# Kernel optimization log

Measured on AMD Instinct MI355X. Metric: run time of the kernel, lower is better.

The kernel has to match this reference:

```python
import jax, jax.numpy as jnp
import numpy as np

HIDDEN = 1024
N_HEADS = 16
HEAD_DIM = HIDDEN // N_HEADS
B, S = 4, 4096


def setup_inputs() -> dict:
    key = jax.random.key(0)
    k1, k2, k3, k4, k5 = jax.random.split(key, 5)
    hidden_states = jax.random.normal(k1, (B, S, HIDDEN), dtype=jnp.float32)
    attention_mask = jnp.zeros((B, 1, 1, S), dtype=jnp.float32)
    scale = 1.0 / np.sqrt(HIDDEN)
    Wq = jax.random.normal(k2, (HIDDEN, HIDDEN), dtype=jnp.float32) * scale
    bq = jax.random.normal(k3, (HIDDEN,), dtype=jnp.float32) * 0.01
    Wkv = jax.random.normal(k4, (HIDDEN, HIDDEN), dtype=jnp.float32) * scale
    bkv = jax.random.normal(k5, (HIDDEN,), dtype=jnp.float32) * 0.01
    return {"hidden_states": hidden_states, "attention_mask": attention_mask,
            "Wq": Wq, "bq": bq, "Wkv": Wkv, "bkv": bkv}


def _split_heads(x, b, s):
    # [B, S, HIDDEN] -> [B, H, S, D]
    return x.reshape(b, s, N_HEADS, HEAD_DIM).transpose(0, 2, 1, 3)


def reference(hidden_states, attention_mask, Wq, bq, Wkv, bkv):
    b, s, _ = hidden_states.shape
    inv_sqrt_d = 1.0 / np.sqrt(HEAD_DIM)

    q = _split_heads(hidden_states @ Wq + bq, b, s)     # [B,H,S,D]
    k = _split_heads(hidden_states @ Wkv + bkv, b, s)   # [B,H,S,D]; value == key

    # ---- global token (index 0) attends to everything ----
    gq = q[:, :, 0:1, :]                                              # [B,H,1,D]
    g_scores = jnp.einsum('bhqd,bhkd->bhqk', gq, k) * inv_sqrt_d + attention_mask
    g_attn = jax.nn.softmax(g_scores, axis=-1)                        # [B,H,1,S]
    g_vec = jnp.einsum('bhqk,bhkd->bhqd', g_attn, k)                  # [B,H,1,D]

    # ---- local tokens 1..S-1: keys = [self, global_vec, prev, next(wrap to 0)] ----
    k_self = k[:, :, 1:, :]                                           # [B,H,S-1,D]
    k_glob = jnp.broadcast_to(g_vec, k_self.shape)                    # [B,H,S-1,D]
    k_prev = k[:, :, :-1, :]                                          # [B,H,S-1,D]
    k_next = jnp.concatenate([k[:, :, 2:, :], k[:, :, 0:1, :]], axis=2)
    keys4 = jnp.stack([k_self, k_glob, k_prev, k_next], axis=-1)      # [B,H,S-1,D,4]

    l_scores = jnp.einsum('bhsd,bhsdk->bhsk', q[:, :, 1:, :], keys4) * inv_sqrt_d
    l_attn = jax.nn.softmax(l_scores, axis=-1)                        # [B,H,S-1,4]
    l_vec = jnp.einsum('bhsk,bhsdk->bhsd', l_attn, keys4)             # [B,H,S-1,D]

    context = jnp.concatenate([g_vec, l_vec], axis=2)                 # [B,H,S,D]
    context = context.transpose(0, 2, 1, 3).reshape(b, s, N_HEADS * HEAD_DIM)
    return context, l_attn[:, :, :, None, :]                          # [B,H,S-1,1,4]
```

## Files before the change

### kernel.cpp

```cpp
#include <hip/hip_runtime.h>
#include <hip/hip_bf16.h>

#define NHEADS 16
#define HDIM   64
#define HID    1024
#define BB     4
#define SS     4096
#define MM     (BB*SS)
#define KK     HID
#define NN     (2*HID)

using short8 = __attribute__((ext_vector_type(8))) short;
using f32x4  = __attribute__((ext_vector_type(4))) float;

__device__ __forceinline__ float bf2f(ushort u) {
  return __uint_as_float(((unsigned)u) << 16);
}
__device__ __forceinline__ ushort f2bf(float f) {
  unsigned u = __float_as_uint(f);
  unsigned r = (u + 0x7fffu + ((u >> 16) & 1u)) >> 16;
  return (ushort)r;
}

__device__ __forceinline__ void gload16(const void* g, void* l) {
  __builtin_amdgcn_global_load_lds(
      (const __attribute__((address_space(1))) void*)g,
      (__attribute__((address_space(3))) void*)l, 16, 0, 0);
}

__global__ __launch_bounds__(256) void cast_hs_k(const float* __restrict__ in,
                                                 ushort* __restrict__ out) {
  size_t i = ((size_t)blockIdx.x * 256 + threadIdx.x) * 8;
  float4 a = *(const float4*)(in + i);
  float4 b = *(const float4*)(in + i + 4);
  ushort r[8];
  r[0]=f2bf(a.x); r[1]=f2bf(a.y); r[2]=f2bf(a.z); r[3]=f2bf(a.w);
  r[4]=f2bf(b.x); r[5]=f2bf(b.y); r[6]=f2bf(b.z); r[7]=f2bf(b.w);
  *(uint4*)(out + i) = *(const uint4*)r;
}

__global__ __launch_bounds__(256) void wcast_k(const float* __restrict__ Wq,
                                               const float* __restrict__ Wkv,
                                               ushort* __restrict__ Bt) {
  __shared__ float tile[32][33];
  int k0 = blockIdx.x * 32, n0 = blockIdx.y * 32;
  int tx = threadIdx.x, ty = threadIdx.y;
  const float* src = (n0 < HID) ? Wq : Wkv;
  int nc = (n0 < HID) ? n0 : n0 - HID;
#pragma unroll
  for (int j = 0; j < 4; ++j)
    tile[ty + 8*j][tx] = src[(size_t)(k0 + ty + 8*j) * HID + nc + tx];
  __syncthreads();
#pragma unroll
  for (int j = 0; j < 4; ++j)
    Bt[(size_t)(n0 + ty + 8*j) * KK + k0 + tx] = f2bf(tile[tx][ty + 8*j]);
}

__global__ __launch_bounds__(512, 2) void gemm_k(const ushort* __restrict__ A,
                                                 const ushort* __restrict__ Bt,
                                                 const float* __restrict__ bq,
                                                 const float* __restrict__ bkv,
                                                 ushort* __restrict__ C) {
  extern __shared__ char lds_c[];
  const int tid = threadIdx.x;
  const int bid = blockIdx.x;
  const int wg = (bid & 7) * 64 + (bid >> 3);
  const int tm = wg >> 3, tn = wg & 7;
  const int w = tid >> 6, lane = tid & 63;
  const int wr = w >> 2, wc = w & 3;
  const int lr = lane & 15, hi = lane >> 4;

  const ushort* Ab = A  + (size_t)tm * 256 * KK;
  const ushort* Bb = Bt + (size_t)tn * 256 * KK;

  const int d0 = tid * 16;
  const int gch = (tid & 3) ^ ((tid >> 3) & 3);
  const size_t soff0 = (size_t)(tid >> 2) * KK + gch * 8;
  const size_t soff1 = soff0 + (size_t)128 * KK;

  const int swz = (hi ^ ((lr >> 1) & 3)) << 4;
  const int arow = (wr * 128 + lr) * 64 + swz;
  const int brow = (wc * 64 + lr) * 64 + swz;

  f32x4 acc[8][4];
#pragma unroll
  for (int M = 0; M < 8; ++M)
#pragma unroll
    for (int n = 0; n < 4; ++n) acc[M][n] = (f32x4){0.f, 0.f, 0.f, 0.f};
  short8 bfrag[4];

#define STG(PANEL, KOFF, DSTB)                                                  \
  {                                                                             \
    const ushort* g_ = (PANEL) + (KOFF);                                        \
    gload16(g_ + soff0, lds_c + (DSTB) + d0);                                   \
    gload16(g_ + soff1, lds_c + (DSTB) + 8192 + d0);                            \
  }

#define LOADB(BBASE)                                                            \
  _Pragma("unroll") for (int n = 0; n < 4; ++n)                                 \
    bfrag[n] = *(const short8*)(lds_c + (BBASE) + n * 1024 + brow);

#define WAITV(N)                                                                \
  { asm volatile("s_waitcnt vmcnt(" #N ")" ::: "memory");                       \
    __builtin_amdgcn_sched_barrier(0); }

#define PH(ABASE, MH, STAGE_CODE, TAIL_CODE)                                    \
  {                                                                             \
    short8 afrag[4];                                                            \
    _Pragma("unroll") for (int m = 0; m < 4; ++m)                               \
      afrag[m] = *(const short8*)(lds_c + (ABASE) + (MH) * 4096 +               \
                                  m * 1024 + arow);                             \
    STAGE_CODE;                                                                 \
    __builtin_amdgcn_s_barrier();                                               \
    __builtin_amdgcn_sched_barrier(0);     \
    __builtin_amdgcn_s_setprio(1);                                              \
    _Pragma("unroll") for (int m = 0; m < 4; ++m)                               \
      _Pragma("unroll") for (int n = 0; n < 4; ++n)                             \
        acc[(MH) * 4 + m][n] = __builtin_amdgcn_mfma_f32_16x16x32_bf16(         \
            bfrag[n], afrag[m], acc[(MH) * 4 + m][n], 0, 0, 0);                 \
    __builtin_amdgcn_s_setprio(0);                                              \
    TAIL_CODE;                                                                  \
    __builtin_amdgcn_s_barrier();                                               \
    asm volatile("" ::: "memory");                                              \
  }

  STG(Bb, 0,   32768);
  STG(Ab, 0,   0);
  STG(Bb, 32,  49152);
  STG(Ab, 32,  16384);
  STG(Bb, 64,  98304);
  STG(Ab, 64,  65536);
  WAITV(8)
  __builtin_amdgcn_s_barrier();
  asm volatile("" ::: "memory");

#pragma unroll 1
  for (int it = 0; it < 7; ++it) {
    LOADB(32768)
    PH(0, 0, STG(Bb, (2 * it + 1) * 64 + 32, 114688), {})
    PH(0, 1, STG(Ab, (2 * it + 1) * 64 + 32, 81920), WAITV(8))
    LOADB(49152)
    PH(16384, 0, STG(Bb, (2 * it + 2) * 64, 32768), {})
    PH(16384, 1, STG(Ab, (2 * it + 2) * 64, 0), WAITV(8))
    LOADB(98304)
    PH(65536, 0, STG(Bb, (2 * it + 2) * 64 + 32, 49152), {})
    PH(65536, 1, STG(Ab, (2 * it + 2) * 64 + 32, 16384), WAITV(8))
    LOADB(114688)
    PH(81920, 0, STG(Bb, (2 * it + 3) * 64, 98304), {})
    PH(81920, 1, STG(Ab, (2 * it + 3) * 64, 65536), WAITV(8))
  }
  LOADB(32768)
  PH(0, 0, STG(Bb, 15 * 64 + 32, 114688), {})
  PH(0, 1, STG(Ab, 15 * 64 + 32, 81920), WAITV(8))
  LOADB(49152)
  PH(16384, 0, {}, {})
  PH(16384, 1, {}, WAITV(4))
  LOADB(98304)
  PH(65536, 0, {}, {})
  PH(65536, 1, {}, WAITV(0))
  LOADB(114688)
  PH(81920, 0, {}, {})
  PH(81920, 1, {}, {})

#undef PH
#undef WAITV
#undef LOADB
#undef STG

  const float* bias = (tn < 4) ? (bq + tn * 256) : (bkv + (tn - 4) * 256);
  float4 bv[4];
#pragma unroll
  for (int n = 0; n < 4; ++n)
    bv[n] = *(const float4*)(bias + wc * 64 + n * 16 + hi * 4);

#pragma unroll
  for (int M = 0; M < 8; ++M) {
    size_t row = (size_t)tm * 256 + wr * 128 + M * 16 + lr;
    ushort* cp = C + row * NN + tn * 256 + wc * 64 + hi * 4;
#pragma unroll
    for (int n = 0; n < 4; ++n) {
      unsigned p0 = (unsigned)f2bf(acc[M][n][0] + bv[n].x) |
                    ((unsigned)f2bf(acc[M][n][1] + bv[n].y) << 16);
      unsigned p1 = (unsigned)f2bf(acc[M][n][2] + bv[n].z) |
                    ((unsigned)f2bf(acc[M][n][3] + bv[n].w) << 16);
      uint2 st; st.x = p0; st.y = p1;
      *(uint2*)(cp + n * 16) = st;
    }
  }
}

#define GCH 8
#define GCS (SS / GCH)

__global__ __launch_bounds__(512) void gattn_part_k(const ushort* __restrict__ QK,
                                                    const float* __restrict__ mask,
                                                    float* __restrict__ P) {
  const int bh = blockIdx.x >> 3, c = blockIdx.x & 7;
  const int b = bh >> 4, h = bh & 15;
  const int tid = threadIdx.x, w = tid >> 6, lane = tid & 63;
  __shared__ float sc[GCS];
  __shared__ float red[8];
  __shared__ float vacc[8][64];

  const float gq = bf2f(QK[(size_t)b * SS * NN + h * HDIM + lane]);
  const int s0 = c * GCS;
  float mx = -1e30f;
  for (int s = w; s < GCS; s += 8) {
    float kv = bf2f(QK[((size_t)b * SS + s0 + s) * NN + HID + h * HDIM + lane]);
    float p = gq * kv;
#pragma unroll
    for (int o = 32; o; o >>= 1) p += __shfl_xor(p, o, 64);
    p = p * 0.125f + mask[b * SS + s0 + s];
    if (lane == 0) sc[s] = p;
    mx = fmaxf(mx, p);
  }
  if (lane == 0) red[w] = mx;
  __syncthreads();
  float bm = -1e30f;
#pragma unroll
  for (int i = 0; i < 8; ++i) bm = fmaxf(bm, red[i]);
  __syncthreads();
  float ls = 0.f;
  for (int s = tid; s < GCS; s += 512) {
    float e = __expf(sc[s] - bm);
    sc[s] = e;
    ls += e;
  }
#pragma unroll
  for (int o = 32; o; o >>= 1) ls += __shfl_xor(ls, o, 64);
  if (lane == 0) red[w] = ls;
  __syncthreads();
  float tot = 0.f;
#pragma unroll
  for (int i = 0; i < 8; ++i) tot += red[i];

  float a = 0.f;
  for (int s = w; s < GCS; s += 8)
    a += sc[s] * bf2f(QK[((size_t)b * SS + s0 + s) * NN + HID + h * HDIM + lane]);
  vacc[w][lane] = a;
  __syncthreads();
  if (w == 0) {
    float v = 0.f;
#pragma unroll
    for (int i = 0; i < 8; ++i) v += vacc[i][lane];
    P[1024 + (bh * 8 + c) * 64 + lane] = v;
    if (lane == 0) {
      P[bh * 8 + c] = bm;
      P[512 + bh * 8 + c] = tot;
    }
  }
}

__global__ __launch_bounds__(64) void gattn_comb_k(const float* __restrict__ P,
                                                   float* __restrict__ ctx,
                                                   float* __restrict__ gvec) {
  const int bh = blockIdx.x, b = bh >> 4, h = bh & 15;
  const int lane = threadIdx.x;
  float pm[8];
  float m = -1e30f;
#pragma unroll
  for (int c = 0; c < 8; ++c) { pm[c] = P[bh * 8 + c]; m = fmaxf(m, pm[c]); }
  float tot = 0.f, g = 0.f;
#pragma unroll
  for (int c = 0; c < 8; ++c) {
    float e = __expf(pm[c] - m);
    tot += P[512 + bh * 8 + c] * e;
    g += P[1024 + (bh * 8 + c) * 64 + lane] * e;
  }
  g /= tot;
  gvec[b * HID + h * HDIM + lane] = g;
  ctx[(size_t)b * SS * HID + h * HDIM + lane] = g;
}

__device__ __forceinline__ void unpack16(const ushort* __restrict__ p, float* f) {
  uint4 v0 = *(const uint4*)p;
  uint4 v1 = *(const uint4*)(p + 8);
  unsigned u[8] = {v0.x, v0.y, v0.z, v0.w, v1.x, v1.y, v1.z, v1.w};
#pragma unroll
  for (int i = 0; i < 8; ++i) {
    f[2*i]   = __uint_as_float(u[i] << 16);
    f[2*i+1] = __uint_as_float(u[i] & 0xffff0000u);
  }
}

__global__ __launch_bounds__(256) void local_attn_k(const ushort* __restrict__ QK,
                                                    const float* __restrict__ gvec,
                                                    float* __restrict__ out) {
  const int blk = blockIdx.x;
  const int b = blk >> 10;
  const int s = 1 + ((blk & 1023) << 2) + (int)(threadIdx.x >> 6);
  if (s >= SS) return;
  const int lane = threadIdx.x & 63;
  const int g = lane >> 2, j = lane & 3;
  const int db = g*HDIM + j*16;

  const size_t base = ((size_t)b*SS + s) * NN;
  const ushort* qp  = QK + base + db;
  const ushort* ksp = QK + base + HID + db;
  const ushort* kpp = QK + base - NN + HID + db;
  const int sn = (s == SS-1) ? 0 : s + 1;
  const ushort* knp = QK + ((size_t)b*SS + sn)*NN + HID + db;
  const float*  gvp = gvec + b*HID + db;

  float q[16], ks[16], kp[16], kn[16], gv[16];
  unpack16(qp, q); unpack16(ksp, ks); unpack16(kpp, kp); unpack16(knp, kn);
#pragma unroll
  for (int t = 0; t < 16; t += 4) *(float4*)(gv + t) = *(const float4*)(gvp + t);

  float d0=0.f, d1=0.f, d2=0.f, d3=0.f;
#pragma unroll
  for (int t = 0; t < 16; ++t) {
    d0 += q[t]*ks[t]; d1 += q[t]*gv[t]; d2 += q[t]*kp[t]; d3 += q[t]*kn[t];
  }
  d0 += __shfl_xor(d0, 1, 64); d0 += __shfl_xor(d0, 2, 64);
  d1 += __shfl_xor(d1, 1, 64); d1 += __shfl_xor(d1, 2, 64);
  d2 += __shfl_xor(d2, 1, 64); d2 += __shfl_xor(d2, 2, 64);
  d3 += __shfl_xor(d3, 1, 64); d3 += __shfl_xor(d3, 2, 64);

  float s0 = d0*0.125f, s1 = d1*0.125f, s2 = d2*0.125f, s3 = d3*0.125f;
  float m = fmaxf(fmaxf(s0, s1), fmaxf(s2, s3));
  float e0 = __expf(s0 - m), e1 = __expf(s1 - m), e2 = __expf(s2 - m), e3 = __expf(s3 - m);
  float inv = 1.f / (e0 + e1 + e2 + e3);
  float a0 = e0*inv, a1 = e1*inv, a2 = e2*inv, a3 = e3*inv;

  float o[16];
#pragma unroll
  for (int t = 0; t < 16; ++t) o[t] = a0*ks[t] + a1*gv[t] + a2*kp[t] + a3*kn[t];
  float* cp = out + ((size_t)b*SS + s)*HID + db;
#pragma unroll
  for (int t = 0; t < 16; t += 4) *(float4*)(cp + t) = *(const float4*)(o + t);

  if (j == 0) {
    float4 av; av.x = a0; av.y = a1; av.z = a2; av.w = a3;
    *(float4*)(out + (size_t)BB*SS*HID + (((size_t)b*NHEADS + g)*(SS-1) + (s-1))*4) = av;
  }
}

extern "C" void kernel_launch(void* const* d_in, const int* in_sizes, int n_in,
                              void* d_out, int out_size, void* d_ws, size_t ws_size,
                              hipStream_t stream) {
  const float* hs   = (const float*)d_in[0];
  const float* mask = (const float*)d_in[1];
  const float* Wq   = (const float*)d_in[2];
  const float* bq   = (const float*)d_in[3];
  const float* Wkv  = (const float*)d_in[4];
  const float* bkv  = (const float*)d_in[5];
  float* out = (float*)d_out;

  char* ws = (char*)d_ws;
  ushort* hsb  = (ushort*)ws;
  ushort* Bt   = (ushort*)(ws + 33554432);
  ushort* QK   = (ushort*)(ws + 33554432 + 4194304);
  float*  gvec = (float*)(ws + 33554432 + 4194304 + 67108864);
  float*  P    = (float*)(ws + 33554432 + 4194304 + 67108864 + 16384);

  cast_hs_k<<<MM*KK/(256*8), 256, 0, stream>>>(hs, hsb);
  wcast_k<<<dim3(KK/32, NN/32), dim3(32, 8), 0, stream>>>(Wq, Wkv, Bt);
  gemm_k<<<dim3((MM/256)*(NN/256)), dim3(512), 131072, stream>>>(hsb, Bt, bq, bkv, QK);
  gattn_part_k<<<BB*NHEADS*GCH, 512, 0, stream>>>(QK, mask, P);
  gattn_comb_k<<<BB*NHEADS, 64, 0, stream>>>(P, out, gvec);
  local_attn_k<<<BB*1024, 256, 0, stream>>>(QK, gvec, out);
}
```

Before: 176.1 us.

## Double-buffer GEMM LDS fragments, fuse cast kernels, cache keys in registers

```diff
diff --git a/kernel.cpp b/kernel.cpp
--- a/kernel.cpp
+++ b/kernel.cpp
@@ -28,32 +28,35 @@
       (__attribute__((address_space(3))) void*)l, 16, 0, 0);
 }
 
-__global__ __launch_bounds__(256) void cast_hs_k(const float* __restrict__ in,
-                                                 ushort* __restrict__ out) {
-  size_t i = ((size_t)blockIdx.x * 256 + threadIdx.x) * 8;
-  float4 a = *(const float4*)(in + i);
-  float4 b = *(const float4*)(in + i + 4);
-  ushort r[8];
-  r[0]=f2bf(a.x); r[1]=f2bf(a.y); r[2]=f2bf(a.z); r[3]=f2bf(a.w);
-  r[4]=f2bf(b.x); r[5]=f2bf(b.y); r[6]=f2bf(b.z); r[7]=f2bf(b.w);
-  *(uint4*)(out + i) = *(const uint4*)r;
-}
-
-__global__ __launch_bounds__(256) void wcast_k(const float* __restrict__ Wq,
-                                               const float* __restrict__ Wkv,
-                                               ushort* __restrict__ Bt) {
+__global__ __launch_bounds__(256) void prep_k(const float* __restrict__ hs,
+                                              const float* __restrict__ Wq,
+                                              const float* __restrict__ Wkv,
+                                              ushort* __restrict__ hsb,
+                                              ushort* __restrict__ Bt) {
   __shared__ float tile[32][33];
-  int k0 = blockIdx.x * 32, n0 = blockIdx.y * 32;
-  int tx = threadIdx.x, ty = threadIdx.y;
-  const float* src = (n0 < HID) ? Wq : Wkv;
-  int nc = (n0 < HID) ? n0 : n0 - HID;
-#pragma unroll
-  for (int j = 0; j < 4; ++j)
-    tile[ty + 8*j][tx] = src[(size_t)(k0 + ty + 8*j) * HID + nc + tx];
-  __syncthreads();
-#pragma unroll
-  for (int j = 0; j < 4; ++j)
-    Bt[(size_t)(n0 + ty + 8*j) * KK + k0 + tx] = f2bf(tile[tx][ty + 8*j]);
+  const int blk = blockIdx.x, tid = threadIdx.x;
+  if (blk < 8192) {
+    size_t i = ((size_t)blk * 256 + tid) * 8;
+    float4 a = *(const float4*)(hs + i);
+    float4 b = *(const float4*)(hs + i + 4);
+    ushort r[8];
+    r[0]=f2bf(a.x); r[1]=f2bf(a.y); r[2]=f2bf(a.z); r[3]=f2bf(a.w);
+    r[4]=f2bf(b.x); r[5]=f2bf(b.y); r[6]=f2bf(b.z); r[7]=f2bf(b.w);
+    *(uint4*)(hsb + i) = *(const uint4*)r;
+  } else {
+    const int e = blk - 8192;
+    const int k0 = (e & 31) * 32, n0 = (e >> 5) * 32;
+    const int tx = tid & 31, ty = tid >> 5;
+    const float* src = (n0 < HID) ? Wq : Wkv;
+    const int nc = (n0 < HID) ? n0 : n0 - HID;
+#pragma unroll
+    for (int j = 0; j < 4; ++j)
+      tile[ty + 8*j][tx] = src[(size_t)(k0 + ty + 8*j) * HID + nc + tx];
+    __syncthreads();
+#pragma unroll
+    for (int j = 0; j < 4; ++j)
+      Bt[(size_t)(n0 + ty + 8*j) * KK + k0 + tx] = f2bf(tile[tx][ty + 8*j]);
+  }
 }
 
 __global__ __launch_bounds__(512, 2) void gemm_k(const ushort* __restrict__ A,
@@ -87,7 +90,8 @@
   for (int M = 0; M < 8; ++M)
 #pragma unroll
     for (int n = 0; n < 4; ++n) acc[M][n] = (f32x4){0.f, 0.f, 0.f, 0.f};
-  short8 bfrag[4];
+
+  short8 aX[4], aY[4], bX[4], bY[4];
 
 #define STG(PANEL, KOFF, DSTB)                                                  \
   {                                                                             \
@@ -96,30 +100,32 @@
     gload16(g_ + soff1, lds_c + (DSTB) + 8192 + d0);                            \
   }
 
-#define LOADB(BBASE)                                                            \
+#define RDA(DST, ABASE, MH)                                                     \
+  _Pragma("unroll") for (int m = 0; m < 4; ++m)                                 \
+    DST[m] = *(const short8*)(lds_c + (ABASE) + (MH) * 4096 + m * 1024 + arow);
+
+#define RDB(DST, BBASE)                                                         \
   _Pragma("unroll") for (int n = 0; n < 4; ++n)                                 \
-    bfrag[n] = *(const short8*)(lds_c + (BBASE) + n * 1024 + brow);
+    DST[n] = *(const short8*)(lds_c + (BBASE) + n * 1024 + brow);
 
 #define WAITV(N)                                                                \
   { asm volatile("s_waitcnt vmcnt(" #N ")" ::: "memory");                       \
     __builtin_amdgcn_sched_barrier(0); }
 
-#define PH(ABASE, MH, STAGE_CODE, TAIL_CODE)                                    \
+#define PHASE(AF, BF, MH, RD_CODE, STG_CODE, WAIT_CODE)                         \
   {                                                                             \
-    short8 afrag[4];                                                            \
-    _Pragma("unroll") for (int m = 0; m < 4; ++m)                               \
-      afrag[m] = *(const short8*)(lds_c + (ABASE) + (MH) * 4096 +               \
-                                  m * 1024 + arow);                             \
-    STAGE_CODE;                                                                 \
+    RD_CODE                                                                     \
+    __builtin_amdgcn_sched_barrier(0);                                          \
+    STG_CODE                                                                    \
     __builtin_amdgcn_s_barrier();                                               \
-    __builtin_amdgcn_sched_barrier(0);     \
+    __builtin_amdgcn_sched_barrier(0);                                          \
     __builtin_amdgcn_s_setprio(1);                                              \
     _Pragma("unroll") for (int m = 0; m < 4; ++m)                               \
       _Pragma("unroll") for (int n = 0; n < 4; ++n)                             \
         acc[(MH) * 4 + m][n] = __builtin_amdgcn_mfma_f32_16x16x32_bf16(         \
-            bfrag[n], afrag[m], acc[(MH) * 4 + m][n], 0, 0, 0);                 \
+            BF[n], AF[m], acc[(MH) * 4 + m][n], 0, 0, 0);                       \
     __builtin_amdgcn_s_setprio(0);                                              \
-    TAIL_CODE;                                                                  \
+    WAIT_CODE                                                                   \
     __builtin_amdgcn_s_barrier();                                               \
     asm volatile("" ::: "memory");                                              \
   }
@@ -130,41 +136,37 @@
   STG(Ab, 32,  16384);
   STG(Bb, 64,  98304);
   STG(Ab, 64,  65536);
-  WAITV(8)
+  WAITV(4)
   __builtin_amdgcn_s_barrier();
   asm volatile("" ::: "memory");
+  RDB(bX, 32768);
+  RDA(aX, 0, 0);
 
 #pragma unroll 1
   for (int it = 0; it < 7; ++it) {
-    LOADB(32768)
-    PH(0, 0, STG(Bb, (2 * it + 1) * 64 + 32, 114688), {})
-    PH(0, 1, STG(Ab, (2 * it + 1) * 64 + 32, 81920), WAITV(8))
-    LOADB(49152)
-    PH(16384, 0, STG(Bb, (2 * it + 2) * 64, 32768), {})
-    PH(16384, 1, STG(Ab, (2 * it + 2) * 64, 0), WAITV(8))
-    LOADB(98304)
-    PH(65536, 0, STG(Bb, (2 * it + 2) * 64 + 32, 49152), {})
-    PH(65536, 1, STG(Ab, (2 * it + 2) * 64 + 32, 16384), WAITV(8))
-    LOADB(114688)
-    PH(81920, 0, STG(Bb, (2 * it + 3) * 64, 98304), {})
-    PH(81920, 1, STG(Ab, (2 * it + 3) * 64, 65536), WAITV(8))
-  }
-  LOADB(32768)
-  PH(0, 0, STG(Bb, 15 * 64 + 32, 114688), {})
-  PH(0, 1, STG(Ab, 15 * 64 + 32, 81920), WAITV(8))
-  LOADB(49152)
-  PH(16384, 0, {}, {})
-  PH(16384, 1, {}, WAITV(4))
-  LOADB(98304)
-  PH(65536, 0, {}, {})
-  PH(65536, 1, {}, WAITV(0))
-  LOADB(114688)
-  PH(81920, 0, {}, {})
-  PH(81920, 1, {}, {})
-
-#undef PH
+    const int t1 = 2 * it + 1, t2 = 2 * it + 2, t3 = 2 * it + 3;
+    PHASE(aX, bX, 0, { RDA(aY, 0, 1); },                      STG(Bb, t1*64+32, 114688), WAITV(6))
+    PHASE(aY, bX, 1, { RDA(aX, 16384, 0); RDB(bY, 49152); },  STG(Ab, t1*64+32, 81920),  WAITV(6))
+    PHASE(aX, bY, 0, { RDA(aY, 16384, 1); },                  STG(Bb, t2*64, 32768),     WAITV(6))
+    PHASE(aY, bY, 1, { RDA(aX, 65536, 0); RDB(bX, 98304); },  STG(Ab, t2*64, 0),         WAITV(6))
+    PHASE(aX, bX, 0, { RDA(aY, 65536, 1); },                  STG(Bb, t2*64+32, 49152),  WAITV(6))
+    PHASE(aY, bX, 1, { RDA(aX, 81920, 0); RDB(bY, 114688); }, STG(Ab, t2*64+32, 16384),  WAITV(6))
+    PHASE(aX, bY, 0, { RDA(aY, 81920, 1); },                  STG(Bb, t3*64, 98304),     WAITV(6))
+    PHASE(aY, bY, 1, { RDA(aX, 0, 0); RDB(bX, 32768); },      STG(Ab, t3*64, 65536),     WAITV(6))
+  }
+  PHASE(aX, bX, 0, { RDA(aY, 0, 1); },                      STG(Bb, 15*64+32, 114688), WAITV(6))
+  PHASE(aY, bX, 1, { RDA(aX, 16384, 0); RDB(bY, 49152); },  STG(Ab, 15*64+32, 81920),  WAITV(6))
+  PHASE(aX, bY, 0, { RDA(aY, 16384, 1); },                  {}, WAITV(4))
+  PHASE(aY, bY, 1, { RDA(aX, 65536, 0); RDB(bX, 98304); },  {}, WAITV(2))
+  PHASE(aX, bX, 0, { RDA(aY, 65536, 1); },                  {}, WAITV(0))
+  PHASE(aY, bX, 1, { RDA(aX, 81920, 0); RDB(bY, 114688); }, {}, {})
+  PHASE(aX, bY, 0, { RDA(aY, 81920, 1); },                  {}, {})
+  PHASE(aY, bY, 1, {}, {}, {})
+
+#undef PHASE
 #undef WAITV
-#undef LOADB
+#undef RDB
+#undef RDA
 #undef STG
 
   const float* bias = (tn < 4) ? (bq + tn * 256) : (bkv + (tn - 4) * 256);
@@ -204,9 +206,13 @@
 
   const float gq = bf2f(QK[(size_t)b * SS * NN + h * HDIM + lane]);
   const int s0 = c * GCS;
+  float kvv[64];
   float mx = -1e30f;
-  for (int s = w; s < GCS; s += 8) {
+#pragma unroll
+  for (int i = 0; i < 64; ++i) {
+    const int s = w + i * 8;
     float kv = bf2f(QK[((size_t)b * SS + s0 + s) * NN + HID + h * HDIM + lane]);
+    kvv[i] = kv;
     float p = gq * kv;
 #pragma unroll
     for (int o = 32; o; o >>= 1) p += __shfl_xor(p, o, 64);
@@ -235,8 +241,8 @@
   for (int i = 0; i < 8; ++i) tot += red[i];
 
   float a = 0.f;
-  for (int s = w; s < GCS; s += 8)
-    a += sc[s] * bf2f(QK[((size_t)b * SS + s0 + s) * NN + HID + h * HDIM + lane]);
+#pragma unroll
+  for (int i = 0; i < 64; ++i) a += sc[w + i * 8] * kvv[i];
   vacc[w][lane] = a;
   __syncthreads();
   if (w == 0) {
@@ -354,8 +360,7 @@
   float*  gvec = (float*)(ws + 33554432 + 4194304 + 67108864);
   float*  P    = (float*)(ws + 33554432 + 4194304 + 67108864 + 16384);
 
-  cast_hs_k<<<MM*KK/(256*8), 256, 0, stream>>>(hs, hsb);
-  wcast_k<<<dim3(KK/32, NN/32), dim3(32, 8), 0, stream>>>(Wq, Wkv, Bt);
+  prep_k<<<8192 + 2048, 256, 0, stream>>>(hs, Wq, Wkv, hsb, Bt);
   gemm_k<<<dim3((MM/256)*(NN/256)), dim3(512), 131072, stream>>>(hsb, Bt, bq, bkv, QK);
   gattn_part_k<<<BB*NHEADS*GCH, 512, 0, stream>>>(QK, mask, P);
   gattn_comb_k<<<BB*NHEADS, 64, 0, stream>>>(P, out, gvec);
```

New measurement: 193.7 us. 10.0% more time.

## Shrink GEMM tiles to 128x128 and reuse neighbor keys in local attention

Applied to the files above, without the earlier changes.

```diff
diff --git a/kernel.cpp b/kernel.cpp
--- a/kernel.cpp
+++ b/kernel.cpp
@@ -56,7 +56,7 @@
     Bt[(size_t)(n0 + ty + 8*j) * KK + k0 + tx] = f2bf(tile[tx][ty + 8*j]);
 }
 
-__global__ __launch_bounds__(512, 2) void gemm_k(const ushort* __restrict__ A,
+__global__ __launch_bounds__(256, 2) void gemm_k(const ushort* __restrict__ A,
                                                  const ushort* __restrict__ Bt,
                                                  const float* __restrict__ bq,
                                                  const float* __restrict__ bkv,
@@ -64,125 +64,117 @@
   extern __shared__ char lds_c[];
   const int tid = threadIdx.x;
   const int bid = blockIdx.x;
-  const int wg = (bid & 7) * 64 + (bid >> 3);
-  const int tm = wg >> 3, tn = wg & 7;
+  const int wg = (bid & 7) * 256 + (bid >> 3);
+  const int tm = wg >> 4, tn = wg & 15;
   const int w = tid >> 6, lane = tid & 63;
-  const int wr = w >> 2, wc = w & 3;
+  const int wr = w >> 1, wc = w & 1;
   const int lr = lane & 15, hi = lane >> 4;
 
-  const ushort* Ab = A  + (size_t)tm * 256 * KK;
-  const ushort* Bb = Bt + (size_t)tn * 256 * KK;
-
-  const int d0 = tid * 16;
-  const int gch = (tid & 3) ^ ((tid >> 3) & 3);
-  const size_t soff0 = (size_t)(tid >> 2) * KK + gch * 8;
-  const size_t soff1 = soff0 + (size_t)128 * KK;
-
-  const int swz = (hi ^ ((lr >> 1) & 3)) << 4;
-  const int arow = (wr * 128 + lr) * 64 + swz;
-  const int brow = (wc * 64 + lr) * 64 + swz;
-
-  f32x4 acc[8][4];
-#pragma unroll
-  for (int M = 0; M < 8; ++M)
-#pragma unroll
-    for (int n = 0; n < 4; ++n) acc[M][n] = (f32x4){0.f, 0.f, 0.f, 0.f};
+  const ushort* Ab = A  + (size_t)tm * 128 * KK;
+  const ushort* Bb = Bt + (size_t)tn * 128 * KK;
+
+  int srow[4], scol[4];
+#pragma unroll
+  for (int i = 0; i < 4; ++i) {
+    int o = i * 4096 + tid * 16;
+    int row = o >> 7, ch = (o >> 4) & 7;
+    srow[i] = row;
+    scol[i] = ((ch ^ (row & 7)) << 3);
+  }
+
+  const int aoff0 = (wr * 64 + lr) * 128;
+  const int boff0 = (wc * 64 + lr) * 128;
+  const int r7 = lr & 7;
+
+  f32x4 acc[4][4];
+#pragma unroll
+  for (int m = 0; m < 4; ++m)
+#pragma unroll
+    for (int n = 0; n < 4; ++n) acc[m][n] = (f32x4){0.f, 0.f, 0.f, 0.f};
   short8 bfrag[4];
 
-#define STG(PANEL, KOFF, DSTB)                                                  \
+#define STGALL(T1, DSTB)                                                        \
   {                                                                             \
-    const ushort* g_ = (PANEL) + (KOFF);                                        \
-    gload16(g_ + soff0, lds_c + (DSTB) + d0);                                   \
-    gload16(g_ + soff1, lds_c + (DSTB) + 8192 + d0);                            \
-  }
-
-#define LOADB(BBASE)                                                            \
+    _Pragma("unroll") for (int i = 0; i < 4; ++i)                               \
+      gload16(Ab + (T1) * 64 + (size_t)srow[i] * KK + scol[i],                  \
+              lds_c + (DSTB) + i * 4096 + tid * 16);                            \
+    _Pragma("unroll") for (int i = 0; i < 4; ++i)                               \
+      gload16(Bb + (T1) * 64 + (size_t)srow[i] * KK + scol[i],                  \
+              lds_c + (DSTB) + 16384 + i * 4096 + tid * 16);                    \
+  }
+
+#define LOADB(BBASE, CB)                                                        \
   _Pragma("unroll") for (int n = 0; n < 4; ++n)                                 \
-    bfrag[n] = *(const short8*)(lds_c + (BBASE) + n * 1024 + brow);
+    bfrag[n] = *(const short8*)(lds_c + (BBASE) + boff0 + n * 2048 +            \
+                                ((((CB) + hi) ^ r7) << 4));
 
 #define WAITV(N)                                                                \
   { asm volatile("s_waitcnt vmcnt(" #N ")" ::: "memory");                       \
     __builtin_amdgcn_sched_barrier(0); }
 
-#define PH(ABASE, MH, STAGE_CODE, TAIL_CODE)                                    \
+#define PH(ABASE, CB, STAGE_CODE, TAIL_CODE)                                    \
   {                                                                             \
     short8 afrag[4];                                                            \
     _Pragma("unroll") for (int m = 0; m < 4; ++m)                               \
-      afrag[m] = *(const short8*)(lds_c + (ABASE) + (MH) * 4096 +               \
-                                  m * 1024 + arow);                             \
+      afrag[m] = *(const short8*)(lds_c + (ABASE) + aoff0 + m * 2048 +          \
+                                  ((((CB) + hi) ^ r7) << 4));                   \
     STAGE_CODE;                                                                 \
     __builtin_amdgcn_s_barrier();                                               \
-    __builtin_amdgcn_sched_barrier(0);     \
+    __builtin_amdgcn_sched_barrier(0);                                          \
     __builtin_amdgcn_s_setprio(1);                                              \
     _Pragma("unroll") for (int m = 0; m < 4; ++m)                               \
       _Pragma("unroll") for (int n = 0; n < 4; ++n)                             \
-        acc[(MH) * 4 + m][n] = __builtin_amdgcn_mfma_f32_16x16x32_bf16(         \
-            bfrag[n], afrag[m], acc[(MH) * 4 + m][n], 0, 0, 0);                 \
+        acc[m][n] = __builtin_amdgcn_mfma_f32_16x16x32_bf16(                    \
+            bfrag[n], afrag[m], acc[m][n], 0, 0, 0);                            \
     __builtin_amdgcn_s_setprio(0);                                              \
     TAIL_CODE;                                                                  \
     __builtin_amdgcn_s_barrier();                                               \
     asm volatile("" ::: "memory");                                              \
   }
 
-  STG(Bb, 0,   32768);
-  STG(Ab, 0,   0);
-  STG(Bb, 32,  49152);
-  STG(Ab, 32,  16384);
-  STG(Bb, 64,  98304);
-  STG(Ab, 64,  65536);
-  WAITV(8)
+  STGALL(0, 0)
+  WAITV(0)
   __builtin_amdgcn_s_barrier();
   asm volatile("" ::: "memory");
 
 #pragma unroll 1
-  for (int it = 0; it < 7; ++it) {
-    LOADB(32768)
-    PH(0, 0, STG(Bb, (2 * it + 1) * 64 + 32, 114688), {})
-    PH(0, 1, STG(Ab, (2 * it + 1) * 64 + 32, 81920), WAITV(8))
-    LOADB(49152)
-    PH(16384, 0, STG(Bb, (2 * it + 2) * 64, 32768), {})
-    PH(16384, 1, STG(Ab, (2 * it + 2) * 64, 0), WAITV(8))
-    LOADB(98304)
-    PH(65536, 0, STG(Bb, (2 * it + 2) * 64 + 32, 49152), {})
-    PH(65536, 1, STG(Ab, (2 * it + 2) * 64 + 32, 16384), WAITV(8))
-    LOADB(114688)
-    PH(81920, 0, STG(Bb, (2 * it + 3) * 64, 98304), {})
-    PH(81920, 1, STG(Ab, (2 * it + 3) * 64, 65536), WAITV(8))
-  }
-  LOADB(32768)
-  PH(0, 0, STG(Bb, 15 * 64 + 32, 114688), {})
-  PH(0, 1, STG(Ab, 15 * 64 + 32, 81920), WAITV(8))
-  LOADB(49152)
-  PH(16384, 0, {}, {})
-  PH(16384, 1, {}, WAITV(4))
-  LOADB(98304)
-  PH(65536, 0, {}, {})
-  PH(65536, 1, {}, WAITV(0))
-  LOADB(114688)
-  PH(81920, 0, {}, {})
-  PH(81920, 1, {}, {})
+  for (int t = 0; t < 15; ++t) {
+    const int cur = (t & 1) << 15;
+    const int alt = cur ^ 32768;
+    LOADB(cur + 16384, 0)
+    PH(cur, 0, STGALL(t + 1, alt), {})
+    LOADB(cur + 16384, 4)
+    PH(cur, 4, {}, WAITV(0))
+  }
+  LOADB(32768 + 16384, 0)
+  PH(32768, 0, {}, {})
+  LOADB(32768 + 16384, 4)
+  PH(32768, 4, {}, {})
 
 #undef PH
 #undef WAITV
 #undef LOADB
-#undef STG
-
-  const float* bias = (tn < 4) ? (bq + tn * 256) : (bkv + (tn - 4) * 256);
+#undef STGALL
+
+  const int colb = tn * 128 + wc * 64;
   float4 bv[4];
 #pragma unroll
-  for (int n = 0; n < 4; ++n)
-    bv[n] = *(const float4*)(bias + wc * 64 + n * 16 + hi * 4);
-
-#pragma unroll
-  for (int M = 0; M < 8; ++M) {
-    size_t row = (size_t)tm * 256 + wr * 128 + M * 16 + lr;
-    ushort* cp = C + row * NN + tn * 256 + wc * 64 + hi * 4;
+  for (int n = 0; n < 4; ++n) {
+    int cg = colb + n * 16 + hi * 4;
+    const float* bias = (cg < HID) ? (bq + cg) : (bkv + cg - HID);
+    bv[n] = *(const float4*)bias;
+  }
+
+#pragma unroll
+  for (int m = 0; m < 4; ++m) {
+    size_t row = (size_t)tm * 128 + wr * 64 + m * 16 + lr;
+    ushort* cp = C + row * NN + colb + hi * 4;
 #pragma unroll
     for (int n = 0; n < 4; ++n) {
-      unsigned p0 = (unsigned)f2bf(acc[M][n][0] + bv[n].x) |
-                    ((unsigned)f2bf(acc[M][n][1] + bv[n].y) << 16);
-      unsigned p1 = (unsigned)f2bf(acc[M][n][2] + bv[n].z) |
-                    ((unsigned)f2bf(acc[M][n][3] + bv[n].w) << 16);
+      unsigned p0 = (unsigned)f2bf(acc[m][n][0] + bv[n].x) |
+                    ((unsigned)f2bf(acc[m][n][1] + bv[n].y) << 16);
+      unsigned p1 = (unsigned)f2bf(acc[m][n][2] + bv[n].z) |
+                    ((unsigned)f2bf(acc[m][n][3] + bv[n].w) << 16);
       uint2 st; st.x = p0; st.y = p1;
       *(uint2*)(cp + n * 16) = st;
     }
@@ -287,52 +279,65 @@
                                                     const float* __restrict__ gvec,
                                                     float* __restrict__ out) {
   const int blk = blockIdx.x;
-  const int b = blk >> 10;
-  const int s = 1 + ((blk & 1023) << 2) + (int)(threadIdx.x >> 6);
-  if (s >= SS) return;
+  const int b = blk >> 8;
+  const int sb = 1 + ((blk & 255) << 4) + ((int)(threadIdx.x >> 6) << 2);
   const int lane = threadIdx.x & 63;
   const int g = lane >> 2, j = lane & 3;
-  const int db = g*HDIM + j*16;
-
-  const size_t base = ((size_t)b*SS + s) * NN;
-  const ushort* qp  = QK + base + db;
-  const ushort* ksp = QK + base + HID + db;
-  const ushort* kpp = QK + base - NN + HID + db;
-  const int sn = (s == SS-1) ? 0 : s + 1;
-  const ushort* knp = QK + ((size_t)b*SS + sn)*NN + HID + db;
-  const float*  gvp = gvec + b*HID + db;
-
-  float q[16], ks[16], kp[16], kn[16], gv[16];
-  unpack16(qp, q); unpack16(ksp, ks); unpack16(kpp, kp); unpack16(knp, kn);
+  const int db = g * HDIM + j * 16;
+
+  float gv[16];
+  const float* gvp = gvec + b * HID + db;
 #pragma unroll
   for (int t = 0; t < 16; t += 4) *(float4*)(gv + t) = *(const float4*)(gvp + t);
 
-  float d0=0.f, d1=0.f, d2=0.f, d3=0.f;
-#pragma unroll
-  for (int t = 0; t < 16; ++t) {
-    d0 += q[t]*ks[t]; d1 += q[t]*gv[t]; d2 += q[t]*kp[t]; d3 += q[t]*kn[t];
-  }
-  d0 += __shfl_xor(d0, 1, 64); d0 += __shfl_xor(d0, 2, 64);
-  d1 += __shfl_xor(d1, 1, 64); d1 += __shfl_xor(d1, 2, 64);
-  d2 += __shfl_xor(d2, 1, 64); d2 += __shfl_xor(d2, 2, 64);
-  d3 += __shfl_xor(d3, 1, 64); d3 += __shfl_xor(d3, 2, 64);
-
-  float s0 = d0*0.125f, s1 = d1*0.125f, s2 = d2*0.125f, s3 = d3*0.125f;
-  float m = fmaxf(fmaxf(s0, s1), fmaxf(s2, s3));
-  float e0 = __expf(s0 - m), e1 = __expf(s1 - m), e2 = __expf(s2 - m), e3 = __expf(s3 - m);
-  float inv = 1.f / (e0 + e1 + e2 + e3);
-  float a0 = e0*inv, a1 = e1*inv, a2 = e2*inv, a3 = e3*inv;
-
-  float o[16];
-#pragma unroll
-  for (int t = 0; t < 16; ++t) o[t] = a0*ks[t] + a1*gv[t] + a2*kp[t] + a3*kn[t];
-  float* cp = out + ((size_t)b*SS + s)*HID + db;
-#pragma unroll
-  for (int t = 0; t < 16; t += 4) *(float4*)(cp + t) = *(const float4*)(o + t);
-
-  if (j == 0) {
-    float4 av; av.x = a0; av.y = a1; av.z = a2; av.w = a3;
-    *(float4*)(out + (size_t)BB*SS*HID + (((size_t)b*NHEADS + g)*(SS-1) + (s-1))*4) = av;
+  float kr[6][16];
+#pragma unroll
+  for (int i = 0; i < 6; ++i) {
+    int R = sb - 1 + i;
+    if (R >= SS) R = 0;
+    unpack16(QK + ((size_t)b * SS + R) * NN + HID + db, kr[i]);
+  }
+
+#pragma unroll
+  for (int p = 0; p < 4; ++p) {
+    const int s = sb + p;
+    if (s >= SS) break;
+    float q[16];
+    unpack16(QK + ((size_t)b * SS + s) * NN + db, q);
+
+    float d0 = 0.f, d1 = 0.f, d2 = 0.f, d3 = 0.f;
+#pragma unroll
+    for (int t = 0; t < 16; ++t) {
+      d0 += q[t] * kr[p + 1][t];
+      d1 += q[t] * gv[t];
+      d2 += q[t] * kr[p][t];
+      d3 += q[t] * kr[p + 2][t];
+    }
+    d0 += __shfl_xor(d0, 1, 64); d0 += __shfl_xor(d0, 2, 64);
+    d1 += __shfl_xor(d1, 1, 64); d1 += __shfl_xor(d1, 2, 64);
+    d2 += __shfl_xor(d2, 1, 64); d2 += __shfl_xor(d2, 2, 64);
+    d3 += __shfl_xor(d3, 1, 64); d3 += __shfl_xor(d3, 2, 64);
+
+    float s0 = d0 * 0.125f, s1 = d1 * 0.125f, s2 = d2 * 0.125f, s3 = d3 * 0.125f;
+    float m = fmaxf(fmaxf(s0, s1), fmaxf(s2, s3));
+    float e0 = __expf(s0 - m), e1 = __expf(s1 - m);
+    float e2 = __expf(s2 - m), e3 = __expf(s3 - m);
+    float inv = 1.f / (e0 + e1 + e2 + e3);
+    float a0 = e0 * inv, a1 = e1 * inv, a2 = e2 * inv, a3 = e3 * inv;
+
+    float o[16];
+#pragma unroll
+    for (int t = 0; t < 16; ++t)
+      o[t] = a0 * kr[p + 1][t] + a1 * gv[t] + a2 * kr[p][t] + a3 * kr[p + 2][t];
+    float* cp = out + ((size_t)b * SS + s) * HID + db;
+#pragma unroll
+    for (int t = 0; t < 16; t += 4) *(float4*)(cp + t) = *(const float4*)(o + t);
+
+    if (j == 0) {
+      float4 av; av.x = a0; av.y = a1; av.z = a2; av.w = a3;
+      *(float4*)(out + (size_t)BB * SS * HID +
+                 (((size_t)b * NHEADS + g) * (SS - 1) + (s - 1)) * 4) = av;
+    }
   }
 }
 
@@ -356,8 +361,8 @@
 
   cast_hs_k<<<MM*KK/(256*8), 256, 0, stream>>>(hs, hsb);
   wcast_k<<<dim3(KK/32, NN/32), dim3(32, 8), 0, stream>>>(Wq, Wkv, Bt);
-  gemm_k<<<dim3((MM/256)*(NN/256)), dim3(512), 131072, stream>>>(hsb, Bt, bq, bkv, QK);
+  gemm_k<<<dim3((MM/128)*(NN/128)), dim3(256), 65536, stream>>>(hsb, Bt, bq, bkv, QK);
   gattn_part_k<<<BB*NHEADS*GCH, 512, 0, stream>>>(QK, mask, P);
   gattn_comb_k<<<BB*NHEADS, 64, 0, stream>>>(P, out, gvec);
-  local_attn_k<<<BB*1024, 256, 0, stream>>>(QK, gvec, out);
-}
+  local_attn_k<<<BB*256, 256, 0, stream>>>(QK, gvec, out);
+}
```

Result: slower. 182.7 us (+3.7%).
